# Performance work log

Hardware: AMD Instinct MI355X
Metric: run time of the kernel (lower is better)

Reference implementation:

```python
import jax, jax.numpy as jnp
import numpy as np

B, NF, FD, ND, C, K, L = 32, 64, 64, 256, 8, 6, 2  # batch, num_frames(feat), fused_dim, nodes, edge channels, neighbors, layers


def setup_inputs() -> dict:
    key = jax.random.key(0)
    ks = jax.random.split(key, 6)
    s = lambda k, shape: jax.random.normal(k, shape, jnp.float32) * 0.05
    return {
        "fused": jax.random.normal(ks[0], (B, NF, FD), jnp.float32),
        "w1": s(ks[1], (NF, FD, FD)),
        "b1": jnp.zeros((NF, 1, FD), jnp.float32),
        "w2": s(ks[2], (NF, FD, ND)),
        "b2": jnp.zeros((NF, 1, ND), jnp.float32),
        "edge_qk_w": s(ks[3], (2 * C * NF, NF)),
        "ga_qk_w": s(ks[4], (L, 2 * NF, NF)),
        "ga_qk_b": jnp.zeros((L, 2 * NF), jnp.float32),
        "ga_w": jnp.ones((L, 1, C), jnp.float32),
    }


def _spec_norm(w):
    # per-node spectral normalization (torch does this in-place under no_grad)
    n = jax.lax.stop_gradient(jnp.linalg.norm(w, ord=2, axis=(1, 2), keepdims=True))
    return w / jnp.clip(n, 1e-6, None)


def _forward(fused, w1, b1, w2, b2, edge_qk_w, ga_qk_w, ga_qk_b, ga_w):
    scale = NF ** -0.5
    # --- MultiNodeMlp (per-frame node-wise MLP) ---
    h = jnp.einsum('bni,nij->bnj', fused, _spec_norm(w1)) + b1[:, 0]
    h = jax.nn.gelu(h, approximate=False)
    conv = jnp.einsum('bni,nio->bno', h, _spec_norm(w2)) + b2[:, 0]  # [B,NF,ND]
    x = conv.transpose(0, 2, 1)  # node features [B,ND,NF]

    # --- EdgeLayer: multi-channel attention + top-k clip + double normalization ---
    qk = (x @ edge_qk_w.T).reshape(B, ND, 2, C, NF)
    q = qk[:, :, 0].transpose(0, 2, 1, 3)  # [B,C,ND,NF]
    k = qk[:, :, 1].transpose(0, 2, 1, 3)
    attn = jax.nn.softmax(jnp.einsum('bcnf,bcmf->bcnm', q, k) * scale, axis=-1)
    sum_edge = jax.lax.stop_gradient(attn).sum(axis=1)            # [B,ND,ND]
    top_idx = jax.lax.top_k(sum_edge, K)[1]                       # [B,ND,K]
    onehot = jnp.clip(jax.nn.one_hot(top_idx, ND, dtype=attn.dtype).sum(axis=2), 0.0, 1.0)
    mask = jnp.maximum(onehot, jnp.eye(ND, dtype=attn.dtype))[:, None]  # [B,1,ND,ND]
    masked = mask * attn
    nr = masked / (masked.sum(-1, keepdims=True) + 1e-6)
    nc = nr / (nr.sum(-2, keepdims=True) + 1e-6)
    edge = jnp.einsum('bcnd,bcmd->bcnm', nr, nc)                  # norm_row @ norm_col^T

    # --- LipschitzGraph: residual invertible graph attention layers ---
    eye = jnp.eye(NF, dtype=x.dtype)
    for l in range(L):
        W, bqk, wch = ga_qk_w[l], ga_qk_b[l], ga_w[l]
        xs = jax.nn.sigmoid(jax.nn.elu(x))
        qkx = xs @ W.T + bqk                                       # [B,ND,2NF]
        qg, kg = qkx[..., :NF], qkx[..., NF:]
        a = jax.nn.softmax(jnp.einsum('bnf,bmf->bnm', qg, kg) * scale, axis=-1)
        ne = a[:, None] * edge                                     # [B,C,ND,ND]
        ne = ne / (ne.sum(-1, keepdims=True) + 1e-6)
        ne = jnp.einsum('bcnd,c->bnd', ne, (wch / wch.sum())[0])
        dot = W[:NF] @ W[NF:].T * scale
        lip = jax.lax.stop_gradient(jnp.linalg.norm(eye + 2.0 * dot, ord=2)) + 5.0
        x = x + (ne @ xs) / lip
    return x


def reference(fused, w1, b1, w2, b2, edge_qk_w, ga_qk_w, ga_qk_b, ga_w):
    return _forward(fused, w1, b1, w2, b2, edge_qk_w, ga_qk_w, ga_qk_b, ga_w)
```

## Files before the change

kernel.cpp:

```cpp
#include <hip/hip_runtime.h>
#include <float.h>
#include <math.h>


typedef short bf8t __attribute__((ext_vector_type(8)));
typedef float f4t __attribute__((ext_vector_type(4)));

static __device__ __forceinline__ unsigned short f2bf(float x) {
  union { float f; unsigned u; } v; v.f = x;
  unsigned r = (v.u + 0x7FFFu + ((v.u >> 16) & 1u)) >> 16;
  return (unsigned short)r;
}
static __device__ __forceinline__ float bf2f(unsigned short s) {
  union { unsigned u; float f; } v; v.u = ((unsigned)s) << 16; return v.f;
}
static __device__ __forceinline__ float bf2f_lo(unsigned u) {
  union { unsigned u; float f; } v; v.u = u << 16; return v.f;
}
static __device__ __forceinline__ float bf2f_hi(unsigned u) {
  union { unsigned u; float f; } v; v.u = u & 0xFFFF0000u; return v.f;
}
static __device__ __forceinline__ float dot3_pair(unsigned uqh, unsigned uql,
                                                  unsigned ukh, unsigned ukl) {
  float s = bf2f_lo(uqh) * (bf2f_lo(ukh) + bf2f_lo(ukl)) + bf2f_lo(uql) * bf2f_lo(ukh);
  s += bf2f_hi(uqh) * (bf2f_hi(ukh) + bf2f_hi(ukl)) + bf2f_hi(uql) * bf2f_hi(ukh);
  return s;
}
static __device__ __forceinline__ void split8(const float* __restrict__ p,
                                              bf8t* hi, bf8t* lo) {
  float4 v0 = *(const float4*)(p);
  float4 v1 = *(const float4*)(p + 4);
  float v[8] = {v0.x, v0.y, v0.z, v0.w, v1.x, v1.y, v1.z, v1.w};
#pragma unroll
  for (int j = 0; j < 8; j++) {
    unsigned short h = f2bf(v[j]);
    (*hi)[j] = (short)h;
    (*lo)[j] = (short)f2bf(v[j] - bf2f(h));
  }
}

#define SPAD 68

static __device__ __forceinline__ void mm_mfma(
    const float* __restrict__ A, const float* __restrict__ B,
    float* __restrict__ C, int t, float scale, int addI, int transposeStore) {
  int wv = t >> 6, l = t & 63;
  int m16 = l & 15, quad = l >> 4;
  bf8t ah[2], al[2];
  const float* ap = A + (size_t)(16 * wv + m16) * SPAD + quad * 8;
  split8(ap, &ah[0], &al[0]);
  split8(ap + 32, &ah[1], &al[1]);
  f4t acc[4];
#pragma unroll
  for (int ct = 0; ct < 4; ct++) {
    bf8t bh[2], bl[2];
    const float* bp = B + (size_t)(ct * 16 + m16) * SPAD + quad * 8;
    split8(bp, &bh[0], &bl[0]);
    split8(bp + 32, &bh[1], &bl[1]);
    f4t a = (f4t){0.f, 0.f, 0.f, 0.f};
    a = __builtin_amdgcn_mfma_f32_16x16x32_bf16(al[0], bh[0], a, 0, 0, 0);
    a = __builtin_amdgcn_mfma_f32_16x16x32_bf16(ah[0], bl[0], a, 0, 0, 0);
    a = __builtin_amdgcn_mfma_f32_16x16x32_bf16(ah[0], bh[0], a, 0, 0, 0);
    a = __builtin_amdgcn_mfma_f32_16x16x32_bf16(al[1], bh[1], a, 0, 0, 0);
    a = __builtin_amdgcn_mfma_f32_16x16x32_bf16(ah[1], bl[1], a, 0, 0, 0);
    a = __builtin_amdgcn_mfma_f32_16x16x32_bf16(ah[1], bh[1], a, 0, 0, 0);
    acc[ct] = a;
  }
#pragma unroll
  for (int ct = 0; ct < 4; ct++)
#pragma unroll
    for (int j = 0; j < 4; j++) {
      int i0 = 16 * wv + quad * 4 + j;
      int j0 = ct * 16 + m16;
      float v = acc[ct][j] * scale + ((addI && i0 == j0) ? 1.0f : 0.0f);
      if (transposeStore) C[(size_t)j0 * SPAD + i0] = v;
      else C[(size_t)i0 * SPAD + j0] = v;
    }
}

static __device__ __forceinline__ void mm_sq_norm(
    const float* __restrict__ A, float* __restrict__ C, int t,
    float* __restrict__ redm) {
  int wv = t >> 6, l = t & 63;
  int m16 = l & 15, quad = l >> 4;
  bf8t ah[2], al[2];
  const float* ap = A + (size_t)(16 * wv + m16) * SPAD + quad * 8;
  split8(ap, &ah[0], &al[0]);
  split8(ap + 32, &ah[1], &al[1]);
  f4t acc[4];
#pragma unroll
  for (int ct = 0; ct < 4; ct++) {
    bf8t bh[2], bl[2];
    const float* bp = A + (size_t)(ct * 16 + m16) * SPAD + quad * 8;
    split8(bp, &bh[0], &bl[0]);
    split8(bp + 32, &bh[1], &bl[1]);
    f4t a = (f4t){0.f, 0.f, 0.f, 0.f};
    a = __builtin_amdgcn_mfma_f32_16x16x32_bf16(al[0], bh[0], a, 0, 0, 0);
    a = __builtin_amdgcn_mfma_f32_16x16x32_bf16(ah[0], bl[0], a, 0, 0, 0);
    a = __builtin_amdgcn_mfma_f32_16x16x32_bf16(ah[0], bh[0], a, 0, 0, 0);
    a = __builtin_amdgcn_mfma_f32_16x16x32_bf16(al[1], bh[1], a, 0, 0, 0);
    a = __builtin_amdgcn_mfma_f32_16x16x32_bf16(ah[1], bl[1], a, 0, 0, 0);
    a = __builtin_amdgcn_mfma_f32_16x16x32_bf16(ah[1], bh[1], a, 0, 0, 0);
    acc[ct] = a;
  }
  float mx = 0.f;
#pragma unroll
  for (int ct = 0; ct < 4; ct++)
#pragma unroll
    for (int j = 0; j < 4; j++) mx = fmaxf(mx, fabsf(acc[ct][j]));
#pragma unroll
  for (int m = 1; m < 64; m <<= 1) mx = fmaxf(mx, __shfl_xor(mx, m, 64));
  if (l == 0) redm[wv] = mx;
  __syncthreads();
  float gmx = fmaxf(fmaxf(redm[0], redm[1]), fmaxf(redm[2], redm[3]));
  float sc = 1.0f / fmaxf(gmx, 1e-30f);
#pragma unroll
  for (int ct = 0; ct < 4; ct++)
#pragma unroll
    for (int j = 0; j < 4; j++)
      C[(size_t)(16 * wv + quad * 4 + j) * SPAD + ct * 16 + m16] = acc[ct][j] * sc;
}

static __device__ __forceinline__ void gram_mfma(
    const float* __restrict__ Ag, int ncols, float* __restrict__ S,
    float* __restrict__ G, int t) {
  int wv = t >> 6, l = t & 63;
  int m16 = l & 15, quad = l >> 4;
  f4t acc[4];
#pragma unroll
  for (int ct = 0; ct < 4; ct++) acc[ct] = (f4t){0.f, 0.f, 0.f, 0.f};
  for (int cc = 0; cc < ncols; cc += 64) {
    if (cc) __syncthreads();
    for (int i = t; i < 1024; i += 256) {
      int r = i >> 4, qq = i & 15;
      float4 v = *(const float4*)(Ag + (size_t)r * ncols + cc + 4 * qq);
      *(float4*)(S + (size_t)r * SPAD + 4 * qq) = v;
    }
    __syncthreads();
    bf8t ah[2], al[2];
    const float* ap = S + (size_t)(16 * wv + m16) * SPAD + quad * 8;
    split8(ap, &ah[0], &al[0]);
    split8(ap + 32, &ah[1], &al[1]);
#pragma unroll
    for (int ct = 0; ct < 4; ct++) {
      bf8t bh[2], bl[2];
      const float* bp = S + (size_t)(ct * 16 + m16) * SPAD + quad * 8;
      split8(bp, &bh[0], &bl[0]);
      split8(bp + 32, &bh[1], &bl[1]);
      f4t a = acc[ct];
      a = __builtin_amdgcn_mfma_f32_16x16x32_bf16(al[0], bh[0], a, 0, 0, 0);
      a = __builtin_amdgcn_mfma_f32_16x16x32_bf16(ah[0], bl[0], a, 0, 0, 0);
      a = __builtin_amdgcn_mfma_f32_16x16x32_bf16(ah[0], bh[0], a, 0, 0, 0);
      a = __builtin_amdgcn_mfma_f32_16x16x32_bf16(al[1], bh[1], a, 0, 0, 0);
      a = __builtin_amdgcn_mfma_f32_16x16x32_bf16(ah[1], bl[1], a, 0, 0, 0);
      a = __builtin_amdgcn_mfma_f32_16x16x32_bf16(ah[1], bh[1], a, 0, 0, 0);
      acc[ct] = a;
    }
  }
  __syncthreads();
#pragma unroll
  for (int ct = 0; ct < 4; ct++)
#pragma unroll
    for (int j = 0; j < 4; j++)
      G[(size_t)(16 * wv + quad * 4 + j) * SPAD + ct * 16 + m16] = acc[ct][j];
}

static __device__ __forceinline__ float power_rayleigh(
    const float* __restrict__ G4m, const float* __restrict__ Gm, int iters, int i) {
  float row[64];
#pragma unroll
  for (int j = 0; j < 16; j++)
    *(float4*)(row + 4 * j) = *(const float4*)(G4m + (size_t)i * SPAD + 4 * j);
  float v = 1.0f + 0.3f * sinf(7.0f * (float)(i + 1));
  for (int it = 0; it < iters; it++) {
    float u0 = 0.f, u1 = 0.f, u2 = 0.f, u3 = 0.f;
#pragma unroll
    for (int j = 0; j < 16; j++) {
      u0 += row[4 * j + 0] * __shfl(v, 4 * j + 0, 64);
      u1 += row[4 * j + 1] * __shfl(v, 4 * j + 1, 64);
      u2 += row[4 * j + 2] * __shfl(v, 4 * j + 2, 64);
      u3 += row[4 * j + 3] * __shfl(v, 4 * j + 3, 64);
    }
    float u = (u0 + u1) + (u2 + u3);
    float ss = u * u;
#pragma unroll
    for (int m = 1; m < 64; m <<= 1) ss += __shfl_xor(ss, m, 64);
    v = u * rsqrtf(fmaxf(ss, 1e-30f));
  }
  float rowg[64];
#pragma unroll
  for (int j = 0; j < 16; j++)
    *(float4*)(rowg + 4 * j) = *(const float4*)(Gm + (size_t)i * SPAD + 4 * j);
  float u0 = 0.f, u1 = 0.f, u2 = 0.f, u3 = 0.f;
#pragma unroll
  for (int j = 0; j < 16; j++) {
    u0 += rowg[4 * j + 0] * __shfl(v, 4 * j + 0, 64);
    u1 += rowg[4 * j + 1] * __shfl(v, 4 * j + 1, 64);
    u2 += rowg[4 * j + 2] * __shfl(v, 4 * j + 2, 64);
    u3 += rowg[4 * j + 3] * __shfl(v, 4 * j + 3, 64);
  }
  float u = (u0 + u1) + (u2 + u3);
  float d = v * u;
#pragma unroll
  for (int m = 1; m < 64; m <<= 1) d += __shfl_xor(d, m, 64);
  return d;
}

__global__ __launch_bounds__(256) void speclip_kernel(
    const float* __restrict__ w1, const float* __restrict__ w2,
    const float* __restrict__ gaw, float* __restrict__ invsig1,
    float* __restrict__ invsig2, float* __restrict__ lipv) {
  __shared__ float Sa[64 * SPAD];
  __shared__ float Sb[64 * SPAD];
  __shared__ float G[64 * SPAD];
  __shared__ float redm[4];
  int t = threadIdx.x;
  int blk = blockIdx.x;
  if (blk < 128) {
    int n = blk & 63;
    const float* A = (blk < 64) ? (w1 + (size_t)n * 4096) : (w2 + (size_t)n * 16384);
    int ncols = (blk < 64) ? 64 : 256;
    gram_mfma(A, ncols, Sa, G, t);
    __syncthreads();
    mm_mfma(G, G, Sa, t, 1.f, 0, 0);
    __syncthreads();
    mm_sq_norm(Sa, Sb, t, redm);  __syncthreads();
    mm_sq_norm(Sb, Sa, t, redm);  __syncthreads();
    mm_sq_norm(Sa, Sb, t, redm);  __syncthreads();
    mm_sq_norm(Sb, Sa, t, redm);  __syncthreads();
    mm_sq_norm(Sa, Sb, t, redm);  __syncthreads();
    mm_sq_norm(Sb, Sa, t, redm);  __syncthreads();
    if (t < 64) {
      float d = power_rayleigh(Sa, G, 2, t);
      if (t == 0) {
        float sg = sqrtf(fmaxf(d, 0.f));
        float inv = 1.0f / fmaxf(sg, 1e-6f);
        if (blk < 64) invsig1[n] = inv; else invsig2[n] = inv;
      }
    }
  } else {
    int l = blk - 128;
    const float* Wb = gaw + (size_t)l * 8192;
    for (int i = t; i < 1024; i += 256) {
      int r = i >> 4, qq = i & 15;
      *(float4*)(Sa + (size_t)r * SPAD + 4 * qq) = *(const float4*)(Wb + r * 64 + 4 * qq);
      *(float4*)(Sb + (size_t)r * SPAD + 4 * qq) = *(const float4*)(Wb + 4096 + r * 64 + 4 * qq);
    }
    __syncthreads();
    mm_mfma(Sa, Sb, G, t, 0.25f, 1, 1);
    __syncthreads();
    mm_mfma(G, G, Sa, t, 1.f, 0, 0);
    __syncthreads();
    mm_sq_norm(Sa, Sb, t, redm);  __syncthreads();
    mm_sq_norm(Sb, G, t, redm);   __syncthreads();
    mm_sq_norm(G, Sb, t, redm);   __syncthreads();
    mm_sq_norm(Sb, G, t, redm);   __syncthreads();
    mm_sq_norm(G, Sb, t, redm);   __syncthreads();
    mm_sq_norm(Sb, G, t, redm);   __syncthreads();
    if (t < 64) {
      float d = power_rayleigh(G, Sa, 2, t);
      if (t == 0) lipv[l] = sqrtf(fmaxf(d, 0.f)) + 5.0f;
    }
  }
}

__global__ __launch_bounds__(256) void hconv_kernel(
    const float* __restrict__ fused, const float* __restrict__ w1,
    const float* __restrict__ b1, const float* __restrict__ invsig1,
    const float* __restrict__ w2, const float* __restrict__ b2,
    const float* __restrict__ invsig2, float* __restrict__ x) {
  __shared__ float fr[256];
  __shared__ float hr[4][64];
  int t = threadIdx.x;
  int blk = blockIdx.x;
  int b = blk >> 4, ng = blk & 15;
  int n0 = ng * 4;
  fr[t] = fused[(size_t)blk * 256 + t];
  __syncthreads();
  {
    int nl = t >> 6, j = t & 63;
    int n = n0 + nl;
    float is1 = invsig1[n];
    const float* fp = fr + nl * 64;
    const float* wp = w1 + (size_t)n * 4096 + j;
    float acc = 0.f;
    for (int i = 0; i < 64; i++) acc += fp[i] * wp[i * 64];
    acc = acc * is1 + b1[n * 64 + j];
    hr[nl][j] = 0.5f * acc * (1.0f + erff(acc * 0.70710678118654752440f));
  }
  __syncthreads();
  const float* w0p = w2 + ((size_t)(n0 + 0) * 64) * 256 + t;
  const float* w1p = w2 + ((size_t)(n0 + 1) * 64) * 256 + t;
  const float* w2p = w2 + ((size_t)(n0 + 2) * 64) * 256 + t;
  const float* w3p = w2 + ((size_t)(n0 + 3) * 64) * 256 + t;
  float a0 = 0.f, a1 = 0.f, a2 = 0.f, a3 = 0.f;
  for (int i = 0; i < 64; i++) {
    a0 += hr[0][i] * w0p[(size_t)i * 256];
    a1 += hr[1][i] * w1p[(size_t)i * 256];
    a2 += hr[2][i] * w2p[(size_t)i * 256];
    a3 += hr[3][i] * w3p[(size_t)i * 256];
  }
  float4 o;
  o.x = a0 * invsig2[n0 + 0] + b2[(n0 + 0) * 256 + t];
  o.y = a1 * invsig2[n0 + 1] + b2[(n0 + 1) * 256 + t];
  o.z = a2 * invsig2[n0 + 2] + b2[(n0 + 2) * 256 + t];
  o.w = a3 * invsig2[n0 + 3] + b2[(n0 + 3) * 256 + t];
  *(float4*)(x + ((size_t)b * 256 + t) * 64 + n0) = o;
}

__global__ __launch_bounds__(256, 2) void qk_kernel(
    const float* __restrict__ x, const float* __restrict__ eqk,
    unsigned short* __restrict__ qhi, unsigned short* __restrict__ qlo,
    unsigned short* __restrict__ khi, unsigned short* __restrict__ klo) {
  int t = threadIdx.x;
  int blk = blockIdx.x;
  int xcd = blk & 7;
  int y = blk >> 3;
  int rh = y & 1;
  int c = (y >> 1) & 7;
  int b = (y >> 4) * 8 + xcd;
  int wv = t >> 6, l = t & 63;
  int m16 = l & 15, quad = l >> 4;
  int row0 = rh * 128 + wv * 32;

  bf8t ah[2][2], al[2][2];
#pragma unroll
  for (int rt = 0; rt < 2; rt++) {
    const float* xp = x + ((size_t)b * 256 + row0 + rt * 16 + m16) * 64 + quad * 8;
    split8(xp, &ah[rt][0], &al[rt][0]);
    split8(xp + 32, &ah[rt][1], &al[rt][1]);
  }
#pragma unroll
  for (int mat = 0; mat < 2; mat++) {
    const float* Wbase = eqk + ((size_t)(mat * 8 + c) * 64) * 64;
    unsigned short* ohi = mat ? khi : qhi;
    unsigned short* olo = mat ? klo : qlo;
#pragma unroll
    for (int ct = 0; ct < 4; ct++) {
      bf8t bh[2], bl[2];
      const float* wp = Wbase + (size_t)(ct * 16 + m16) * 64 + quad * 8;
      split8(wp, &bh[0], &bl[0]);
      split8(wp + 32, &bh[1], &bl[1]);
#pragma unroll
      for (int rt = 0; rt < 2; rt++) {
        f4t a = (f4t){0.f, 0.f, 0.f, 0.f};
        a = __builtin_amdgcn_mfma_f32_16x16x32_bf16(al[rt][0], bh[0], a, 0, 0, 0);
        a = __builtin_amdgcn_mfma_f32_16x16x32_bf16(ah[rt][0], bl[0], a, 0, 0, 0);
        a = __builtin_amdgcn_mfma_f32_16x16x32_bf16(ah[rt][0], bh[0], a, 0, 0, 0);
        a = __builtin_amdgcn_mfma_f32_16x16x32_bf16(al[rt][1], bh[1], a, 0, 0, 0);
        a = __builtin_amdgcn_mfma_f32_16x16x32_bf16(ah[rt][1], bl[1], a, 0, 0, 0);
        a = __builtin_amdgcn_mfma_f32_16x16x32_bf16(ah[rt][1], bh[1], a, 0, 0, 0);
#pragma unroll
        for (int j = 0; j < 4; j++) {
          int n = row0 + rt * 16 + quad * 4 + j;
          int f = ct * 16 + m16;
          size_t o = (((size_t)b * 8 + c) * 256 + n) * 64 + f;
          float v = a[j];
          unsigned short hh = f2bf(v);
          ohi[o] = hh;
          olo[o] = f2bf(v - bf2f(hh));
        }
      }
    }
  }
}

__global__ __launch_bounds__(512, 4) void attn_kernel(
    const unsigned short* __restrict__ qhi, const unsigned short* __restrict__ qlo,
    const unsigned short* __restrict__ khi, const unsigned short* __restrict__ klo,
    float* __restrict__ seP, float* __restrict__ mxb, float* __restrict__ rzb) {
  __shared__ uint4 KS4[4096];
  unsigned short* KS = (unsigned short*)KS4;
  float* sE = (float*)KS4;
  int t = threadIdx.x;
  int blk = blockIdx.x;
  int xcd = blk & 7;
  int y = blk >> 3;
  int b = xcd * 4 + (y & 3);
  int cg = (y >> 2) & 3;
  int ng = y >> 4;
  int wave = t >> 6;
  int ci = wave >> 2;
  int wv = wave & 3;
  int l = t & 63;
  int m16 = l & 15, quad = l >> 4;
  int n0w = ng * 64 + wv * 16;
  int c = cg * 2 + ci;

  size_t slA = ((size_t)b * 8 + cg * 2) * 16384;
  size_t slB = slA + 16384;
  size_t sl = ((size_t)b * 8 + c) * 16384;

  const bf8t* qh = (const bf8t*)(qhi + sl + (size_t)(n0w + m16) * 64 + quad * 8);
  const bf8t* ql = (const bf8t*)(qlo + sl + (size_t)(n0w + m16) * 64 + quad * 8);
  bf8t ah0 = qh[0], ah1 = qh[4];
  bf8t al0 = ql[0], al1 = ql[4];

  int sthalf = (t >> 6) & 1;
  int tllo = (t >> 7) & 3;
  int srcbase = tllo * 1024 + m16 * 64 + sthalf * 32 + quad * 8;
  int dstbase = t * 8;

  int lane8 = (quad * 16 + m16) * 8;
  int cbase = ci * 16384;

  f4t acc[16];
#pragma unroll
  for (int mt = 0; mt < 16; mt++) acc[mt] = (f4t){0.f, 0.f, 0.f, 0.f};

#pragma unroll
  for (int p = 0; p < 2; p++) {
    if (p) __syncthreads();
    int pb = srcbase + p * 8192;
#pragma unroll
    for (int g = 0; g < 2; g++) {
      const unsigned short* bhp = khi + (g ? slB : slA) + pb;
      const unsigned short* blp = klo + (g ? slB : slA) + pb;
      uint4 v0 = *(const uint4*)(bhp);
      uint4 v1 = *(const uint4*)(bhp + 4096);
      uint4 v2 = *(const uint4*)(blp);
      uint4 v3 = *(const uint4*)(blp + 4096);
      *(uint4*)(KS + dstbase + (g * 4 + 0) * 4096) = v0;
      *(uint4*)(KS + dstbase + (g * 4 + 1) * 4096) = v1;
      *(uint4*)(KS + dstbase + (g * 4 + 2) * 4096) = v2;
      *(uint4*)(KS + dstbase + (g * 4 + 3) * 4096) = v3;
    }
    __syncthreads();
#pragma unroll
    for (int tl = 0; tl < 8; tl++) {
      int mt = p * 8 + tl;
      int tb = cbase + tl * 1024 + lane8;
      bf8t bh0 = *(const bf8t*)(KS + tb);
      bf8t bh1 = *(const bf8t*)(KS + tb + 512);
      bf8t bl0 = *(const bf8t*)(KS + tb + 8192);
      bf8t bl1 = *(const bf8t*)(KS + tb + 8704);
      f4t a = acc[mt];
      a = __builtin_amdgcn_mfma_f32_16x16x32_bf16(al0, bh0, a, 0, 0, 0);
      a = __builtin_amdgcn_mfma_f32_16x16x32_bf16(ah0, bl0, a, 0, 0, 0);
      a = __builtin_amdgcn_mfma_f32_16x16x32_bf16(ah0, bh0, a, 0, 0, 0);
      a = __builtin_amdgcn_mfma_f32_16x16x32_bf16(al1, bh1, a, 0, 0, 0);
      a = __builtin_amdgcn_mfma_f32_16x16x32_bf16(ah1, bl1, a, 0, 0, 0);
      a = __builtin_amdgcn_mfma_f32_16x16x32_bf16(ah1, bh1, a, 0, 0, 0);
      acc[mt] = a;
    }
  }
#pragma unroll
  for (int j = 0; j < 4; j++) {
    float mx = -FLT_MAX;
#pragma unroll
    for (int mt = 0; mt < 16; mt++) mx = fmaxf(mx, acc[mt][j]);
    mx = fmaxf(mx, __shfl_xor(mx, 1, 64));
    mx = fmaxf(mx, __shfl_xor(mx, 2, 64));
    mx = fmaxf(mx, __shfl_xor(mx, 4, 64));
    mx = fmaxf(mx, __shfl_xor(mx, 8, 64));
    float mxl = mx * 0.125f;
    float z = 0.f;
#pragma unroll
    for (int mt = 0; mt < 16; mt++) {
      float e = expf(acc[mt][j] * 0.125f - mxl);
      acc[mt][j] = e;
      z += e;
    }
    z += __shfl_xor(z, 1, 64);
    z += __shfl_xor(z, 2, 64);
    z += __shfl_xor(z, 4, 64);
    z += __shfl_xor(z, 8, 64);
    int n = n0w + quad * 4 + j;
    if (m16 == 0) {
      mxb[((size_t)b * 8 + c) * 256 + n] = mxl;
      rzb[((size_t)b * 8 + c) * 256 + n] = z;
    }
    float zi = 1.0f / z;
#pragma unroll
    for (int mt = 0; mt < 16; mt++) acc[mt][j] *= zi;
  }
  __syncthreads();
  for (int half = 0; half < 2; half++) {
    if (ci == 0 && (wv >> 1) == half) {
      int r0 = (wv & 1) * 16;
#pragma unroll
      for (int mt = 0; mt < 16; mt++)
#pragma unroll
        for (int j = 0; j < 4; j++)
          sE[(r0 + quad * 4 + j) * 260 + mt * 16 + m16] = acc[mt][j];
    }
    __syncthreads();
    if (ci == 1 && (wv >> 1) == half) {
      int r0 = (wv & 1) * 16;
#pragma unroll
      for (int mt = 0; mt < 16; mt++)
#pragma unroll
        for (int j = 0; j < 4; j++)
          sE[(r0 + quad * 4 + j) * 260 + mt * 16 + m16] += acc[mt][j];
    }
    __syncthreads();
    float4* dst4 = (float4*)(seP + (((size_t)cg * 32 + b) * 256 + ng * 64 + half * 32) * 256);
    for (int i = t; i < 2048; i += 512) {
      int r = i >> 6, c4 = i & 63;
      dst4[i] = *(const float4*)(sE + r * 260 + c4 * 4);
    }
    if (half == 0) __syncthreads();
  }
}

__global__ __launch_bounds__(256) void topsel_kernel(
    const float* __restrict__ seP, int* __restrict__ idx7) {
  __shared__ float seL[64 * 260];
  __shared__ float cv[64][24];
  __shared__ int cidx[64][24];
  int t = threadIdx.x;
  int b = blockIdx.x >> 2, rg = blockIdx.x & 3;
  int n0 = rg * 64;
  const float* s0 = seP + ((size_t)b * 256 + n0) * 256;
  const float* s1 = seP + ((size_t)(32 + b) * 256 + n0) * 256;
  const float* s2 = seP + ((size_t)(64 + b) * 256 + n0) * 256;
  const float* s3 = seP + ((size_t)(96 + b) * 256 + n0) * 256;
  for (int i = t; i < 4096; i += 256) {
    int m4 = i & 63, r = i >> 6;
    float4 v0 = ((const float4*)(s0 + (size_t)r * 256))[m4];
    float4 v1 = ((const float4*)(s1 + (size_t)r * 256))[m4];
    float4 v2 = ((const float4*)(s2 + (size_t)r * 256))[m4];
    float4 v3 = ((const float4*)(s3 + (size_t)r * 256))[m4];
    float4 s;
    s.x = (v0.x + v1.x) + (v2.x + v3.x);
    s.y = (v0.y + v1.y) + (v2.y + v3.y);
    s.z = (v0.z + v1.z) + (v2.z + v3.z);
    s.w = (v0.w + v1.w) + (v2.w + v3.w);
    *(float4*)(seL + r * 260 + m4 * 4) = s;
  }
  __syncthreads();
  {
    int r = t >> 2, qtr = t & 3;
    float tv[6]; int ti[6];
#pragma unroll
    for (int s = 0; s < 6; s++) { tv[s] = -FLT_MAX; ti[s] = 1 << 30; }
    for (int i = 0; i < 64; i++) {
      int m = 4 * i + qtr;
      float val = seL[r * 260 + m];
      if (val > tv[5]) {
        tv[5] = val; ti[5] = m;
#pragma unroll
        for (int s = 5; s > 0; s--) {
          if (tv[s] > tv[s - 1]) {
            float tmv = tv[s]; tv[s] = tv[s - 1]; tv[s - 1] = tmv;
            int tmi = ti[s]; ti[s] = ti[s - 1]; ti[s - 1] = tmi;
          }
        }
      }
    }
#pragma unroll
    for (int s = 0; s < 6; s++) { cv[r][qtr * 6 + s] = tv[s]; cidx[r][qtr * 6 + s] = ti[s]; }
  }
  __syncthreads();
  if (t < 64) {
    int r = t, n = n0 + r;
    int sel[7];
    for (int round = 0; round < 6; round++) {
      float best = -FLT_MAX; int bi = 1 << 30, bs = 0;
      for (int j = 0; j < 24; j++) {
        float v = cv[r][j]; int id = cidx[r][j];
        if (v > best || (v == best && id < bi)) { best = v; bi = id; bs = j; }
      }
      sel[round] = bi;
      cv[r][bs] = -FLT_MAX;
    }
    bool dup = false;
#pragma unroll
    for (int j = 0; j < 6; j++) dup = dup || (sel[j] == n);
    sel[6] = dup ? -1 : n;
#pragma unroll
    for (int j = 0; j < 7; j++) idx7[((size_t)b * 256 + n) * 7 + j] = sel[j];
  }
}

__global__ __launch_bounds__(256) void nr_kernel(
    const unsigned short* __restrict__ qhi, const unsigned short* __restrict__ qlo,
    const unsigned short* __restrict__ khi, const unsigned short* __restrict__ klo,
    const float* __restrict__ mxb, const float* __restrict__ rzb,
    const int* __restrict__ idx7, float* __restrict__ nrv,
    float* __restrict__ colsum) {
  __shared__ int idxs[7];
  __shared__ float attL[56];
  int t = threadIdx.x;
  int b = blockIdx.x >> 8, n = blockIdx.x & 255;
  if (t < 7) idxs[t] = idx7[(size_t)blockIdx.x * 7 + t];
  __syncthreads();
  int task = t >> 2, l4 = t & 3;
  if (task < 56) {
    int c = task / 7, j = task - c * 7;
    int d = idxs[j];
    float s = 0.f;
    if (d >= 0) {
      size_t qo = (((size_t)b * 8 + c) * 256 + n) * 64 + l4 * 16;
      size_t ko = (((size_t)b * 8 + c) * 256 + d) * 64 + l4 * 16;
      const uint4* qh4 = (const uint4*)(qhi + qo);
      const uint4* ql4 = (const uint4*)(qlo + qo);
      const uint4* kh4 = (const uint4*)(khi + ko);
      const uint4* kl4 = (const uint4*)(klo + ko);
#pragma unroll
      for (int g = 0; g < 2; g++) {
        uint4 uqh = qh4[g], uql = ql4[g], ukh = kh4[g], ukl = kl4[g];
        s += dot3_pair(uqh.x, uql.x, ukh.x, ukl.x);
        s += dot3_pair(uqh.y, uql.y, ukh.y, ukl.y);
        s += dot3_pair(uqh.z, uql.z, ukh.z, ukl.z);
        s += dot3_pair(uqh.w, uql.w, ukh.w, ukl.w);
      }
    }
    s += __shfl_xor(s, 1, 64);
    s += __shfl_xor(s, 2, 64);
    if (l4 == 0) {
      float att = 0.f;
      if (d >= 0) {
        float logit = s * 0.125f;
        att = expf(logit - mxb[((size_t)b * 8 + c) * 256 + n]) / rzb[((size_t)b * 8 + c) * 256 + n];
      }
      attL[task] = att;
    }
  }
  __syncthreads();
  if (t < 8) {
    float rs = 0.f;
#pragma unroll
    for (int j = 0; j < 7; j++) rs += attL[t * 7 + j];
    float ri = 1.0f / (rs + 1e-6f);
#pragma unroll
    for (int j = 0; j < 7; j++) {
      float nv = attL[t * 7 + j] * ri;
      nrv[(((size_t)b * 8 + t) * 256 + n) * 7 + j] = nv;
      int d = idxs[j];
      if (d >= 0) atomicAdd(&colsum[((size_t)b * 8 + t) * 256 + d], nv);
    }
  }
}

__global__ __launch_bounds__(256, 3) void edge_kernel(
    const int* __restrict__ idx7, const float* __restrict__ nrv,
    const float* __restrict__ colsum, unsigned short* __restrict__ edge) {
  __shared__ unsigned short ncT[256 * 64];
  __shared__ short idxL[256 * 8];
  __shared__ float nrvL[256 * 8];
  int t = threadIdx.x;
  int blk = blockIdx.x;
  int b = blk >> 5, c = (blk >> 2) & 7, mq = blk & 3;
  int m0 = mq * 64;
  for (int i = t; i < 8192; i += 256) ((unsigned int*)ncT)[i] = 0u;
  for (int i = t; i < 2048; i += 256) {
    int r = i >> 3, j = i & 7;
    if (j < 7) {
      idxL[i] = (short)idx7[(size_t)b * 1792 + r * 7 + j];
      nrvL[i] = nrv[((size_t)b * 8 + c) * 1792 + r * 7 + j];
    } else {
      idxL[i] = -1;
      nrvL[i] = 0.f;
    }
  }
  __syncthreads();
  for (int i = t; i < 448; i += 256) {
    int mi = i / 7, j = i - mi * 7;
    int m = m0 + mi;
    int d = idxL[m * 8 + j];
    if (d >= 0) {
      float cs = colsum[((size_t)b * 8 + c) * 256 + d];
      ncT[d * 64 + mi] = f2bf(nrvL[m * 8 + j] / (cs + 1e-6f));
    }
  }
  __syncthreads();
  int wv = t >> 6, l = t & 63;
  int half = l >> 5, p = l & 31;
  const unsigned int* ncP = (const unsigned int*)ncT;
  unsigned int* eb = (unsigned int*)(edge + (((size_t)b * 8 + c) * 256) * 256);
  for (int nn = 0; nn < 32; nn++) {
    int n = nn * 8 + wv * 2 + half;
    int4 iv = *(const int4*)(idxL + n * 8);
    float4 w0 = *(const float4*)(nrvL + n * 8);
    float4 w1 = *(const float4*)(nrvL + n * 8 + 4);
    float a0 = 0.f, a1 = 0.f;
    int d;
    unsigned int pr;
    d = (int)(short)(iv.x & 0xFFFF);
    if (d >= 0) { pr = ncP[d * 32 + p]; a0 += w0.x * bf2f_lo(pr); a1 += w0.x * bf2f_hi(pr); }
    d = iv.x >> 16;
    if (d >= 0) { pr = ncP[d * 32 + p]; a0 += w0.y * bf2f_lo(pr); a1 += w0.y * bf2f_hi(pr); }
    d = (int)(short)(iv.y & 0xFFFF);
    if (d >= 0) { pr = ncP[d * 32 + p]; a0 += w0.z * bf2f_lo(pr); a1 += w0.z * bf2f_hi(pr); }
    d = iv.y >> 16;
    if (d >= 0) { pr = ncP[d * 32 + p]; a0 += w0.w * bf2f_lo(pr); a1 += w0.w * bf2f_hi(pr); }
    d = (int)(short)(iv.z & 0xFFFF);
    if (d >= 0) { pr = ncP[d * 32 + p]; a0 += w1.x * bf2f_lo(pr); a1 += w1.x * bf2f_hi(pr); }
    d = iv.z >> 16;
    if (d >= 0) { pr = ncP[d * 32 + p]; a0 += w1.y * bf2f_lo(pr); a1 += w1.y * bf2f_hi(pr); }
    d = (int)(short)(iv.w & 0xFFFF);
    if (d >= 0) { pr = ncP[d * 32 + p]; a0 += w1.z * bf2f_lo(pr); a1 += w1.z * bf2f_hi(pr); }
    unsigned int packo = (unsigned int)f2bf(a0) | ((unsigned int)f2bf(a1) << 16);
    eb[n * 128 + (m0 >> 1) + p] = packo;
  }
}

static __device__ __forceinline__ float selu1(float v) {
  float e = (v > 0.f) ? v : expm1f(v);
  return 1.0f / (1.0f + expf(-e));
}
__global__ __launch_bounds__(256, 1) void qkx_kernel(
    const float* __restrict__ x, const float* __restrict__ gaw,
    const float* __restrict__ gab, int l, float* __restrict__ xs,
    float* __restrict__ qg, float* __restrict__ kgT) {
  __shared__ float xsL[64 * 64];
  __shared__ float kT[64][65];
  int t = threadIdx.x;
  int b = blockIdx.x >> 2, nt = blockIdx.x & 3;
  int f = t & 63, part = t >> 6;
  float wq[64], wk[64];
  const float4* Wq4 = (const float4*)(gaw + (size_t)l * 8192 + f * 64);
  const float4* Wk4 = (const float4*)(gaw + (size_t)l * 8192 + (64 + f) * 64);
#pragma unroll
  for (int j = 0; j < 16; j++) {
    float4 aa = Wq4[j];
    wq[4 * j + 0] = aa.x; wq[4 * j + 1] = aa.y; wq[4 * j + 2] = aa.z; wq[4 * j + 3] = aa.w;
    float4 bb = Wk4[j];
    wk[4 * j + 0] = bb.x; wk[4 * j + 1] = bb.y; wk[4 * j + 2] = bb.z; wk[4 * j + 3] = bb.w;
  }
  float bq = gab[l * 128 + f], bk = gab[l * 128 + 64 + f];
  for (int i = t; i < 1024; i += 256) {
    float4 v = ((const float4*)(x + ((size_t)b * 256 + nt * 64) * 64))[i];
    float4 o;
    o.x = selu1(v.x); o.y = selu1(v.y); o.z = selu1(v.z); o.w = selu1(v.w);
    ((float4*)xsL)[i] = o;
    ((float4*)(xs + ((size_t)b * 256 + nt * 64) * 64))[i] = o;
  }
  __syncthreads();
  for (int i = 0; i < 16; i++) {
    int nl = part * 16 + i;
    const float4* xr = (const float4*)(xsL + nl * 64);
    float aq = 0.f, ak = 0.f;
#pragma unroll
    for (int j = 0; j < 16; j++) {
      float4 v = xr[j];
      aq += v.x * wq[4 * j] + v.y * wq[4 * j + 1] + v.z * wq[4 * j + 2] + v.w * wq[4 * j + 3];
      ak += v.x * wk[4 * j] + v.y * wk[4 * j + 1] + v.z * wk[4 * j + 2] + v.w * wk[4 * j + 3];
    }
    int n = nt * 64 + nl;
    qg[((size_t)b * 256 + n) * 64 + f] = aq + bq;
    kT[f][nl] = ak + bk;
  }
  __syncthreads();
  for (int i = t; i < 1024; i += 256) {
    int ff = i >> 4, qq = i & 15;
    float4 o;
    o.x = kT[ff][4 * qq + 0];
    o.y = kT[ff][4 * qq + 1];
    o.z = kT[ff][4 * qq + 2];
    o.w = kT[ff][4 * qq + 3];
    *(float4*)(kgT + (size_t)b * 16384 + ff * 256 + nt * 64 + 4 * qq) = o;
  }
}

__global__ __launch_bounds__(256, 2) void ga_attn_kernel(
    const float* __restrict__ qg, const float* __restrict__ kgT,
    float* __restrict__ a) {
  int t = threadIdx.x;
  int b = blockIdx.x >> 3, nt = blockIdx.x & 7;
  int n0 = nt * 32;
  int wv = t >> 6, l = t & 63;
  const float* kb = kgT + (size_t)b * 16384 + 4 * l;
  const float* qb = qg + ((size_t)b * 256 + n0 + wv * 8) * 64;
  float acc[8][4];
#pragma unroll
  for (int r = 0; r < 8; r++)
#pragma unroll
    for (int j = 0; j < 4; j++) acc[r][j] = 0.f;
#pragma unroll 4
  for (int kq4 = 0; kq4 < 64; kq4 += 4) {
    float4 kv0 = *(const float4*)(kb + (kq4 + 0) * 256);
    float4 kv1 = *(const float4*)(kb + (kq4 + 1) * 256);
    float4 kv2 = *(const float4*)(kb + (kq4 + 2) * 256);
    float4 kv3 = *(const float4*)(kb + (kq4 + 3) * 256);
#pragma unroll
    for (int r = 0; r < 8; r++) {
      float4 qv = *(const float4*)(qb + r * 64 + kq4);
      acc[r][0] += qv.x * kv0.x + qv.y * kv1.x + qv.z * kv2.x + qv.w * kv3.x;
      acc[r][1] += qv.x * kv0.y + qv.y * kv1.y + qv.z * kv2.y + qv.w * kv3.y;
      acc[r][2] += qv.x * kv0.z + qv.y * kv1.z + qv.z * kv2.z + qv.w * kv3.z;
      acc[r][3] += qv.x * kv0.w + qv.y * kv1.w + qv.z * kv2.w + qv.w * kv3.w;
    }
  }
#pragma unroll
  for (int r = 0; r < 8; r++) {
    float l0 = acc[r][0] * 0.125f, l1 = acc[r][1] * 0.125f;
    float l2 = acc[r][2] * 0.125f, l3 = acc[r][3] * 0.125f;
    float mx = fmaxf(fmaxf(l0, l1), fmaxf(l2, l3));
#pragma unroll
    for (int m = 1; m < 64; m <<= 1) mx = fmaxf(mx, __shfl_xor(mx, m, 64));
    float e0 = expf(l0 - mx), e1 = expf(l1 - mx), e2 = expf(l2 - mx), e3 = expf(l3 - mx);
    float z = e0 + e1 + e2 + e3;
#pragma unroll
    for (int m = 1; m < 64; m <<= 1) z += __shfl_xor(z, m, 64);
    float zi = 1.0f / z;
    int n = n0 + wv * 8 + r;
    float4 o;
    o.x = e0 * zi; o.y = e1 * zi; o.z = e2 * zi; o.w = e3 * zi;
    ((float4*)(a + ((size_t)b * 256 + n) * 256))[l] = o;
  }
}

__global__ __launch_bounds__(256) void upd_kernel(
    const float* __restrict__ a, const unsigned short* __restrict__ edge,
    const float* __restrict__ xs, const float* __restrict__ gaww,
    const float* __restrict__ lipv, int l, float* __restrict__ x) {
  __shared__ float tt[4][8][260];
  __shared__ float ne3[4][256];
  __shared__ float parts[4][4][64];
  __shared__ float dred[32][8];
  __shared__ float dinv[4][8];
  __shared__ float wcL[8];
  __shared__ float lipi;
  int t = threadIdx.x;
  int b = blockIdx.x >> 6, nq = blockIdx.x & 63;
  int n0 = nq * 4;
  if (t == 0) {
    float s = 0.f;
    float wtmp[8];
    for (int c = 0; c < 8; c++) { wtmp[c] = gaww[l * 8 + c]; s += wtmp[c]; }
    for (int c = 0; c < 8; c++) wcL[c] = wtmp[c] / s;
    lipi = 1.0f / lipv[l];
  }
#pragma unroll
  for (int r = 0; r < 4; r++) {
    float av = a[((size_t)b * 256 + n0 + r) * 256 + t];
#pragma unroll
    for (int c = 0; c < 8; c++)
      tt[r][c][t] = av * bf2f(edge[(((size_t)b * 8 + c) * 256 + n0 + r) * 256 + t]);
  }
  __syncthreads();
  {
    int rc = t >> 3, i = t & 7;
    int r = rc >> 3, c = rc & 7;
    float p = 0.f;
#pragma unroll
    for (int kq = 0; kq < 32; kq++) p += tt[r][c][i + 8 * kq];
    dred[rc][i] = p;
  }
  __syncthreads();
  if (t < 32) {
    float s = 0.f;
#pragma unroll
    for (int i = 0; i < 8; i++) s += dred[t][i];
    dinv[t >> 3][t & 7] = 1.0f / (s + 1e-6f);
  }
  __syncthreads();
#pragma unroll
  for (int r = 0; r < 4; r++) {
    float s = 0.f;
#pragma unroll
    for (int c = 0; c < 8; c++) s += wcL[c] * tt[r][c][t] * dinv[r][c];
    ne3[r][t] = s;
  }
  __syncthreads();
  {
    int f = t & 63, part = t >> 6;
    float a0 = 0.f, a1 = 0.f, a2 = 0.f, a3 = 0.f;
    for (int mm = 0; mm < 64; mm++) {
      int m = part * 64 + mm;
      float xv = xs[((size_t)b * 256 + m) * 64 + f];
      a0 += ne3[0][m] * xv;
      a1 += ne3[1][m] * xv;
      a2 += ne3[2][m] * xv;
      a3 += ne3[3][m] * xv;
    }
    parts[0][part][f] = a0;
    parts[1][part][f] = a1;
    parts[2][part][f] = a2;
    parts[3][part][f] = a3;
  }
  __syncthreads();
  {
    int r = t >> 6, f = t & 63;
    float dx = parts[r][0][f] + parts[r][1][f] + parts[r][2][f] + parts[r][3][f];
    x[((size_t)b * 256 + n0 + r) * 64 + f] += dx * lipi;
  }
}

extern "C" void kernel_launch(void* const* d_in, const int* in_sizes, int n_in,
                              void* d_out, int out_size, void* d_ws, size_t ws_size,
                              hipStream_t stream) {
  (void)in_sizes; (void)n_in; (void)out_size; (void)ws_size;
  const float* fused = (const float*)d_in[0];
  const float* w1 = (const float*)d_in[1];
  const float* b1 = (const float*)d_in[2];
  const float* w2 = (const float*)d_in[3];
  const float* b2 = (const float*)d_in[4];
  const float* eqk = (const float*)d_in[5];
  const float* gaw = (const float*)d_in[6];
  const float* gab = (const float*)d_in[7];
  const float* gaww = (const float*)d_in[8];
  float* x = (float*)d_out;
  char* ws = (char*)d_ws;
  size_t off = 0;
  auto alloc = [&](size_t bytes) -> char* {
    char* p = ws + off;
    off += (bytes + 1023) & ~(size_t)1023;
    return p;
  };
  float* invsig1 = (float*)alloc(64 * 4);
  float* invsig2 = (float*)alloc(64 * 4);
  float* lipv = (float*)alloc(2 * 4);
  unsigned short* qhi = (unsigned short*)alloc((size_t)32 * 8 * 256 * 64 * 2);
  unsigned short* qlo = (unsigned short*)alloc((size_t)32 * 8 * 256 * 64 * 2);
  unsigned short* khi = (unsigned short*)alloc((size_t)32 * 8 * 256 * 64 * 2);
  unsigned short* klo = (unsigned short*)alloc((size_t)32 * 8 * 256 * 64 * 2);
  char* sep_edge = alloc((size_t)4 * 32 * 256 * 256 * 4);
  float* seP = (float*)sep_edge;
  unsigned short* edge = (unsigned short*)sep_edge;
  float* mxb = (float*)alloc((size_t)65536 * 4);
  float* rzb = (float*)alloc((size_t)65536 * 4);
  int* idx7 = (int*)alloc((size_t)8192 * 7 * 4);
  float* nrv = (float*)alloc((size_t)65536 * 7 * 4);
  float* colsum = (float*)alloc((size_t)65536 * 4);
  float* xs = (float*)alloc((size_t)524288 * 4);
  float* qg = (float*)alloc((size_t)524288 * 4);
  float* a = (float*)alloc((size_t)32 * 256 * 256 * 4);
  float* kgT = (float*)alloc((size_t)524288 * 4);

  speclip_kernel<<<130, 256, 0, stream>>>(w1, w2, gaw, invsig1, invsig2, lipv);
  hconv_kernel<<<512, 256, 0, stream>>>(fused, w1, b1, invsig1, w2, b2, invsig2, x);
  qk_kernel<<<512, 256, 0, stream>>>(x, eqk, qhi, qlo, khi, klo);
  attn_kernel<<<512, 512, 0, stream>>>(qhi, qlo, khi, klo, seP, mxb, rzb);
  hipMemsetAsync(colsum, 0, (size_t)65536 * 4, stream);
  topsel_kernel<<<128, 256, 0, stream>>>(seP, idx7);
  nr_kernel<<<8192, 256, 0, stream>>>(qhi, qlo, khi, klo, mxb, rzb, idx7, nrv, colsum);
  edge_kernel<<<1024, 256, 0, stream>>>(idx7, nrv, colsum, edge);
  for (int l = 0; l < 2; l++) {
    qkx_kernel<<<128, 256, 0, stream>>>(x, gaw, gab, l, xs, qg, kgT);
    ga_attn_kernel<<<256, 256, 0, stream>>>(qg, kgT, a);
    upd_kernel<<<2048, 256, 0, stream>>>(a, edge, xs, gaww, lipv, l, x);
  }
}
```

Before: 366.4 us.

## Fuse graph-attention softmax into update kernel, drop attention matrix buffer

Removes the separate ga_attn_kernel and computes the 4-row q·k logits and softmax inside upd_kernel, with block-wide max and sum reductions through shared memory. This avoids writing and re-reading the 32x256x256 fp32 attention matrix and saves one launch per layer. kg is now stored row-major, so the transpose in qkx_kernel goes away. In exchange, each upd block reads the whole per-batch kg (256x64) and recomputes dot products, and it adds extra barriers.

```diff
diff --git a/kernel.cpp b/kernel.cpp
--- a/kernel.cpp
+++ b/kernel.cpp
@@ -703,9 +703,8 @@
 __global__ __launch_bounds__(256, 1) void qkx_kernel(
     const float* __restrict__ x, const float* __restrict__ gaw,
     const float* __restrict__ gab, int l, float* __restrict__ xs,
-    float* __restrict__ qg, float* __restrict__ kgT) {
+    float* __restrict__ qg, float* __restrict__ kg) {
   __shared__ float xsL[64 * 64];
-  __shared__ float kT[64][65];
   int t = threadIdx.x;
   int b = blockIdx.x >> 2, nt = blockIdx.x & 3;
   int f = t & 63, part = t >> 6;
@@ -740,70 +739,13 @@
     }
     int n = nt * 64 + nl;
     qg[((size_t)b * 256 + n) * 64 + f] = aq + bq;
-    kT[f][nl] = ak + bk;
-  }
-  __syncthreads();
-  for (int i = t; i < 1024; i += 256) {
-    int ff = i >> 4, qq = i & 15;
-    float4 o;
-    o.x = kT[ff][4 * qq + 0];
-    o.y = kT[ff][4 * qq + 1];
-    o.z = kT[ff][4 * qq + 2];
-    o.w = kT[ff][4 * qq + 3];
-    *(float4*)(kgT + (size_t)b * 16384 + ff * 256 + nt * 64 + 4 * qq) = o;
-  }
-}
-
-__global__ __launch_bounds__(256, 2) void ga_attn_kernel(
-    const float* __restrict__ qg, const float* __restrict__ kgT,
-    float* __restrict__ a) {
-  int t = threadIdx.x;
-  int b = blockIdx.x >> 3, nt = blockIdx.x & 7;
-  int n0 = nt * 32;
-  int wv = t >> 6, l = t & 63;
-  const float* kb = kgT + (size_t)b * 16384 + 4 * l;
-  const float* qb = qg + ((size_t)b * 256 + n0 + wv * 8) * 64;
-  float acc[8][4];
-#pragma unroll
-  for (int r = 0; r < 8; r++)
-#pragma unroll
-    for (int j = 0; j < 4; j++) acc[r][j] = 0.f;
-#pragma unroll 4
-  for (int kq4 = 0; kq4 < 64; kq4 += 4) {
-    float4 kv0 = *(const float4*)(kb + (kq4 + 0) * 256);
-    float4 kv1 = *(const float4*)(kb + (kq4 + 1) * 256);
-    float4 kv2 = *(const float4*)(kb + (kq4 + 2) * 256);
-    float4 kv3 = *(const float4*)(kb + (kq4 + 3) * 256);
-#pragma unroll
-    for (int r = 0; r < 8; r++) {
-      float4 qv = *(const float4*)(qb + r * 64 + kq4);
-      acc[r][0] += qv.x * kv0.x + qv.y * kv1.x + qv.z * kv2.x + qv.w * kv3.x;
-      acc[r][1] += qv.x * kv0.y + qv.y * kv1.y + qv.z * kv2.y + qv.w * kv3.y;
-      acc[r][2] += qv.x * kv0.z + qv.y * kv1.z + qv.z * kv2.z + qv.w * kv3.z;
-      acc[r][3] += qv.x * kv0.w + qv.y * kv1.w + qv.z * kv2.w + qv.w * kv3.w;
-    }
-  }
-#pragma unroll
-  for (int r = 0; r < 8; r++) {
-    float l0 = acc[r][0] * 0.125f, l1 = acc[r][1] * 0.125f;
-    float l2 = acc[r][2] * 0.125f, l3 = acc[r][3] * 0.125f;
-    float mx = fmaxf(fmaxf(l0, l1), fmaxf(l2, l3));
-#pragma unroll
-    for (int m = 1; m < 64; m <<= 1) mx = fmaxf(mx, __shfl_xor(mx, m, 64));
-    float e0 = expf(l0 - mx), e1 = expf(l1 - mx), e2 = expf(l2 - mx), e3 = expf(l3 - mx);
-    float z = e0 + e1 + e2 + e3;
-#pragma unroll
-    for (int m = 1; m < 64; m <<= 1) z += __shfl_xor(z, m, 64);
-    float zi = 1.0f / z;
-    int n = n0 + wv * 8 + r;
-    float4 o;
-    o.x = e0 * zi; o.y = e1 * zi; o.z = e2 * zi; o.w = e3 * zi;
-    ((float4*)(a + ((size_t)b * 256 + n) * 256))[l] = o;
+    kg[((size_t)b * 256 + n) * 64 + f] = ak + bk;
   }
 }
 
 __global__ __launch_bounds__(256) void upd_kernel(
-    const float* __restrict__ a, const unsigned short* __restrict__ edge,
+    const float* __restrict__ qg, const float* __restrict__ kg,
+    const unsigned short* __restrict__ edge,
     const float* __restrict__ xs, const float* __restrict__ gaww,
     const float* __restrict__ lipv, int l, float* __restrict__ x) {
   __shared__ float tt[4][8][260];
@@ -813,9 +755,12 @@
   __shared__ float dinv[4][8];
   __shared__ float wcL[8];
   __shared__ float lipi;
+  __shared__ float qgL[4][64];
+  __shared__ float rred[2][4][4];
   int t = threadIdx.x;
   int b = blockIdx.x >> 6, nq = blockIdx.x & 63;
   int n0 = nq * 4;
+  int wave = t >> 6;
   if (t == 0) {
     float s = 0.f;
     float wtmp[8];
@@ -823,12 +768,76 @@
     for (int c = 0; c < 8; c++) wcL[c] = wtmp[c] / s;
     lipi = 1.0f / lipv[l];
   }
+  {
+    int r = t >> 6, f = t & 63;
+    qgL[r][f] = qg[((size_t)b * 256 + n0 + r) * 64 + f];
+  }
+  __syncthreads();
+  float d0 = 0.f, d1 = 0.f, d2 = 0.f, d3 = 0.f;
+  {
+    const float4* kr = (const float4*)(kg + ((size_t)b * 256 + t) * 64);
+#pragma unroll
+    for (int j = 0; j < 16; j++) {
+      float4 kv = kr[j];
+      float4 q0 = ((const float4*)qgL[0])[j];
+      float4 q1 = ((const float4*)qgL[1])[j];
+      float4 q2 = ((const float4*)qgL[2])[j];
+      float4 q3 = ((const float4*)qgL[3])[j];
+      d0 += q0.x * kv.x + q0.y * kv.y + q0.z * kv.z + q0.w * kv.w;
+      d1 += q1.x * kv.x + q1.y * kv.y + q1.z * kv.z + q1.w * kv.w;
+      d2 += q2.x * kv.x + q2.y * kv.y + q2.z * kv.z + q2.w * kv.w;
+      d3 += q3.x * kv.x + q3.y * kv.y + q3.z * kv.z + q3.w * kv.w;
+    }
+  }
+  d0 *= 0.125f; d1 *= 0.125f; d2 *= 0.125f; d3 *= 0.125f;
+  {
+    float m0 = d0, m1 = d1, m2 = d2, m3 = d3;
+#pragma unroll
+    for (int mm = 1; mm < 64; mm <<= 1) {
+      m0 = fmaxf(m0, __shfl_xor(m0, mm, 64));
+      m1 = fmaxf(m1, __shfl_xor(m1, mm, 64));
+      m2 = fmaxf(m2, __shfl_xor(m2, mm, 64));
+      m3 = fmaxf(m3, __shfl_xor(m3, mm, 64));
+    }
+    if ((t & 63) == 0) {
+      rred[0][0][wave] = m0; rred[0][1][wave] = m1;
+      rred[0][2][wave] = m2; rred[0][3][wave] = m3;
+    }
+  }
+  __syncthreads();
+  {
+    float g0 = fmaxf(fmaxf(rred[0][0][0], rred[0][0][1]), fmaxf(rred[0][0][2], rred[0][0][3]));
+    float g1 = fmaxf(fmaxf(rred[0][1][0], rred[0][1][1]), fmaxf(rred[0][1][2], rred[0][1][3]));
+    float g2 = fmaxf(fmaxf(rred[0][2][0], rred[0][2][1]), fmaxf(rred[0][2][2], rred[0][2][3]));
+    float g3 = fmaxf(fmaxf(rred[0][3][0], rred[0][3][1]), fmaxf(rred[0][3][2], rred[0][3][3]));
+    d0 = expf(d0 - g0); d1 = expf(d1 - g1); d2 = expf(d2 - g2); d3 = expf(d3 - g3);
+    float s0 = d0, s1 = d1, s2 = d2, s3 = d3;
+#pragma unroll
+    for (int mm = 1; mm < 64; mm <<= 1) {
+      s0 += __shfl_xor(s0, mm, 64);
+      s1 += __shfl_xor(s1, mm, 64);
+      s2 += __shfl_xor(s2, mm, 64);
+      s3 += __shfl_xor(s3, mm, 64);
+    }
+    if ((t & 63) == 0) {
+      rred[1][0][wave] = s0; rred[1][1][wave] = s1;
+      rred[1][2][wave] = s2; rred[1][3][wave] = s3;
+    }
+  }
+  __syncthreads();
+  float av[4];
+  {
+    float z0 = (rred[1][0][0] + rred[1][0][1]) + (rred[1][0][2] + rred[1][0][3]);
+    float z1 = (rred[1][1][0] + rred[1][1][1]) + (rred[1][1][2] + rred[1][1][3]);
+    float z2 = (rred[1][2][0] + rred[1][2][1]) + (rred[1][2][2] + rred[1][2][3]);
+    float z3 = (rred[1][3][0] + rred[1][3][1]) + (rred[1][3][2] + rred[1][3][3]);
+    av[0] = d0 / z0; av[1] = d1 / z1; av[2] = d2 / z2; av[3] = d3 / z3;
+  }
 #pragma unroll
   for (int r = 0; r < 4; r++) {
-    float av = a[((size_t)b * 256 + n0 + r) * 256 + t];
 #pragma unroll
     for (int c = 0; c < 8; c++)
-      tt[r][c][t] = av * bf2f(edge[(((size_t)b * 8 + c) * 256 + n0 + r) * 256 + t]);
+      tt[r][c][t] = av[r] * bf2f(edge[(((size_t)b * 8 + c) * 256 + n0 + r) * 256 + t]);
   }
   __syncthreads();
   {
@@ -917,8 +926,7 @@
   float* colsum = (float*)alloc((size_t)65536 * 4);
   float* xs = (float*)alloc((size_t)524288 * 4);
   float* qg = (float*)alloc((size_t)524288 * 4);
-  float* a = (float*)alloc((size_t)32 * 256 * 256 * 4);
-  float* kgT = (float*)alloc((size_t)524288 * 4);
+  float* kg = (float*)alloc((size_t)524288 * 4);
 
   speclip_kernel<<<130, 256, 0, stream>>>(w1, w2, gaw, invsig1, invsig2, lipv);
   hconv_kernel<<<512, 256, 0, stream>>>(fused, w1, b1, invsig1, w2, b2, invsig2, x);
@@ -929,8 +937,7 @@
   nr_kernel<<<8192, 256, 0, stream>>>(qhi, qlo, khi, klo, mxb, rzb, idx7, nrv, colsum);
   edge_kernel<<<1024, 256, 0, stream>>>(idx7, nrv, colsum, edge);
   for (int l = 0; l < 2; l++) {
-    qkx_kernel<<<128, 256, 0, stream>>>(x, gaw, gab, l, xs, qg, kgT);
-    ga_attn_kernel<<<256, 256, 0, stream>>>(qg, kgT, a);
-    upd_kernel<<<2048, 256, 0, stream>>>(a, edge, xs, gaww, lipv, l, x);
-  }
-}
+    qkx_kernel<<<128, 256, 0, stream>>>(x, gaw, gab, l, xs, qg, kg);
+    upd_kernel<<<2048, 256, 0, stream>>>(qg, kg, edge, xs, gaww, lipv, l, x);
+  }
+}
```

Result: no change. 367.6 us (+0.3%).
